# Performance work log

Hardware: AMD Instinct MI355X
Metric: run time of the kernel (lower is better)

## Reference

```python
import jax, jax.numpy as jnp
import numpy as np

SEQ, BATCH, IN = 512, 256, 15
H1, H2, FC_HID, NUM_CLASSES = 512, 512, 64, 1


def setup_inputs() -> dict:
    key = jax.random.key(0)
    ks = jax.random.split(key, 14)
    def u(k, shape, fan_in):
        b = 1.0 / np.sqrt(fan_in)
        return jax.random.uniform(k, shape, jnp.float32, -b, b)
    return {
        "x": jax.random.normal(ks[0], (SEQ, BATCH, IN), jnp.float32),
        # PyTorch LSTM params, gate order i,f,g,o stacked along dim 0
        "W_ih1": u(ks[1], (4 * H1, IN), H1),
        "W_hh1": u(ks[2], (4 * H1, H1), H1),
        "b_ih1": u(ks[3], (4 * H1,), H1),
        "b_hh1": u(ks[4], (4 * H1,), H1),
        "W_ih2": u(ks[5], (4 * H2, H1), H2),
        "W_hh2": u(ks[6], (4 * H2, H2), H2),
        "b_ih2": u(ks[7], (4 * H2,), H2),
        "b_hh2": u(ks[8], (4 * H2,), H2),
        "fc1_w": u(ks[9], (FC_HID, H2), H2),
        "fc1_b": u(ks[10], (FC_HID,), H2),
        "fc_w": u(ks[11], (NUM_CLASSES, FC_HID), FC_HID),
        "fc_b": u(ks[12], (NUM_CLASSES,), FC_HID),
    }


def _lstm_cell(x_t, h, c, W_ih, W_hh, b_ih, b_hh):
    # gates: [B, 4H], PyTorch gate order i, f, g, o
    g = x_t @ W_ih.T + b_ih + h @ W_hh.T + b_hh
    i, f, gg, o = jnp.split(g, 4, axis=-1)
    c_new = jax.nn.sigmoid(f) * c + jax.nn.sigmoid(i) * jnp.tanh(gg)
    h_new = jax.nn.sigmoid(o) * jnp.tanh(c_new)
    return h_new, c_new


def reference(x, W_ih1, W_hh1, b_ih1, b_hh1, W_ih2, W_hh2, b_ih2, b_hh2,
              fc1_w, fc1_b, fc_w, fc_b):
    S, B, _ = x.shape
    init = (jnp.zeros((B, H1), x.dtype), jnp.zeros((B, H1), x.dtype),
            jnp.zeros((B, H2), x.dtype), jnp.zeros((B, H2), x.dtype))

    def step(carry, x_t):
        h1, c1, h2, c2 = carry
        h1, c1 = _lstm_cell(x_t, h1, c1, W_ih1, W_hh1, b_ih1, b_hh1)
        h2, c2 = _lstm_cell(h1, h2, c2, W_ih2, W_hh2, b_ih2, b_hh2)
        return (h1, c1, h2, c2), None

    (h1, c1, h2, c2), _ = jax.lax.scan(step, init, x)
    # MLP head on final-timestep top-layer hidden state; `out += out` doubles it
    hn = jax.nn.relu(h2)
    out = jax.nn.relu(hn @ fc1_w.T + fc1_b)
    out = out @ fc_w.T + fc_b
    return out + out
```

## Files before the change

kernel.cpp:

```cpp
#include <hip/hip_runtime.h>
#include <cstdint>
#include <cstddef>

typedef __attribute__((ext_vector_type(8))) short short8;
typedef __attribute__((ext_vector_type(4))) float floatx4;

constexpr int kSeq = 512;
constexpr int kBatch = 256;
constexpr int kIn = 15;
constexpr int kH = 512;
constexpr int kG = 4 * kH;
constexpr size_t kHSlot = (size_t)kBatch * kH;
constexpr size_t kShmemBytes = 131072 + 4096;

__device__ __forceinline__ unsigned short f2bf(float f) {
    union { float f; unsigned u; } v; v.f = f;
    unsigned u = v.u;
    return (unsigned short)((u + 0x7fffu + ((u >> 16) & 1u)) >> 16);
}

__device__ __forceinline__ float sigm(float x) { return 1.0f / (1.0f + __expf(-x)); }
__device__ __forceinline__ float tanh_(float x) { return 1.0f - 2.0f / (1.0f + __expf(2.0f * x)); }

#define LLC_LOAD16(A, P)                                                      \
    asm volatile(                                                             \
        "global_load_dwordx4 %0, %16, off sc0 sc1\n\t"                        \
        "global_load_dwordx4 %1, %16, off offset:64 sc0 sc1\n\t"              \
        "global_load_dwordx4 %2, %16, off offset:128 sc0 sc1\n\t"             \
        "global_load_dwordx4 %3, %16, off offset:192 sc0 sc1\n\t"             \
        "global_load_dwordx4 %4, %16, off offset:256 sc0 sc1\n\t"             \
        "global_load_dwordx4 %5, %16, off offset:320 sc0 sc1\n\t"             \
        "global_load_dwordx4 %6, %16, off offset:384 sc0 sc1\n\t"             \
        "global_load_dwordx4 %7, %16, off offset:448 sc0 sc1\n\t"             \
        "global_load_dwordx4 %8, %16, off offset:512 sc0 sc1\n\t"             \
        "global_load_dwordx4 %9, %16, off offset:576 sc0 sc1\n\t"             \
        "global_load_dwordx4 %10, %16, off offset:640 sc0 sc1\n\t"            \
        "global_load_dwordx4 %11, %16, off offset:704 sc0 sc1\n\t"            \
        "global_load_dwordx4 %12, %16, off offset:768 sc0 sc1\n\t"            \
        "global_load_dwordx4 %13, %16, off offset:832 sc0 sc1\n\t"            \
        "global_load_dwordx4 %14, %16, off offset:896 sc0 sc1\n\t"            \
        "global_load_dwordx4 %15, %16, off offset:960 sc0 sc1\n\t"            \
        "s_waitcnt vmcnt(0)"                                                  \
        : "=&v"((A)[0]), "=&v"((A)[1]), "=&v"((A)[2]), "=&v"((A)[3]),         \
          "=&v"((A)[4]), "=&v"((A)[5]), "=&v"((A)[6]), "=&v"((A)[7]),         \
          "=&v"((A)[8]), "=&v"((A)[9]), "=&v"((A)[10]), "=&v"((A)[11]),       \
          "=&v"((A)[12]), "=&v"((A)[13]), "=&v"((A)[14]), "=&v"((A)[15])      \
        : "v"(P) : "memory")

#define LLC_STORE16(P, V)                                                     \
    asm volatile("global_store_dwordx4 %0, %1, off sc0 sc1"                   \
                 :: "v"(P), "v"(V) : "memory")

__device__ __forceinline__ void waitf(const int* flags, int tgt, int lane, int& fc) {
    if (tgt <= 0) return;
    bool watch = (lane < 32);
    if (__all(!watch || fc >= tgt)) return;
    for (;;) {
        if (watch && fc < tgt)
            fc = __hip_atomic_load(flags + lane * 16,
                                   __ATOMIC_RELAXED, __HIP_MEMORY_SCOPE_AGENT);
        if (__all(!watch || fc >= tgt)) return;
        __builtin_amdgcn_s_sleep(1);
    }
}

__global__ void k_conv(const float* __restrict__ src, unsigned short* __restrict__ dst, int n) {
    int i = blockIdx.x * blockDim.x + threadIdx.x;
    if (i < n) dst[i] = f2bf(src[i]);
}

__global__ void k_conv_pad(const float* __restrict__ src, unsigned short* __restrict__ dst, int rows) {
    int i = blockIdx.x * blockDim.x + threadIdx.x;
    if (i >= rows * 32) return;
    int r = i >> 5, k = i & 31;
    dst[i] = (k < kIn) ? f2bf(src[r * kIn + k]) : (unsigned short)0;
}

__global__ __launch_bounds__(256) void k_persist(
    const unsigned short* __restrict__ whh1b,
    const unsigned short* __restrict__ wih1b,
    const unsigned short* __restrict__ wih2b,
    const unsigned short* __restrict__ whh2b,
    const unsigned short* __restrict__ xb,
    const float* __restrict__ bih1, const float* __restrict__ bhh1,
    const float* __restrict__ bih2, const float* __restrict__ bhh2,
    unsigned short* __restrict__ h1r,
    unsigned short* __restrict__ h2r,
    float* __restrict__ h2f,
    int* __restrict__ flags)
{
    extern __shared__ unsigned short lw[];
    const int bid = blockIdx.x;
    const int g = bid & 3;
    const int role = bid >> 2;
    const bool is2 = role >= 32;
    const int rid = role & 31;
    const int j0 = rid << 4;
    const int tid = (int)threadIdx.x;
    const int wave = tid >> 6;
    const int lane = tid & 63;
    const int lcol = lane & 15;
    const int quad = lane >> 4;
    const int m0 = (g << 6) + wave * 16;
    const int arow = m0 + lcol;
    const int koff = quad * 8;

    int* f1 = flags + g * 1024;
    int* f2 = f1 + 512;
    int* myflag = (is2 ? f2 : f1) + rid * 16;
    unsigned short* scr = lw + 65536 + wave * 384;

    if (!is2) {
        for (int i = tid; i < 4096; i += 256) {
            int ln = i >> 6, gg = ln >> 4, u = ln & 15;
            int c = i & 63, kk = c >> 2, qd = c & 3;
            *(short8*)&lw[((gg * 16 + kk) << 9) + ((qd * 16 + u) << 3)] =
                *(const short8*)&whh1b[(size_t)((gg << 9) + j0 + u) * kH + c * 8];
        }
        for (int i = tid; i < 256; i += 256) {
            int ln = i >> 2, gg = ln >> 4, u = ln & 15;
            int qd = i & 3;
            *(short8*)&lw[((64 + gg) << 9) + ((qd * 16 + u) << 3)] =
                *(const short8*)&wih1b[((gg << 9) + j0 + u) * 32 + qd * 8];
        }
    } else {
        for (int i = tid; i < 4096; i += 256) {
            int ln = i >> 6, gg = ln >> 4, u = ln & 15;
            int c = i & 63, kk = c >> 2, qd = c & 3;
            int dst = ((gg * 16 + kk) << 9) + ((qd * 16 + u) << 3);
            size_t src = (size_t)((gg << 9) + j0 + u) * kH + c * 8;
            *(short8*)&lw[dst] = *(const short8*)&wih2b[src];
            *(short8*)&lw[dst + (64 << 9)] = *(const short8*)&whh2b[src];
        }
    }
    float bsum[4];
#pragma unroll
    for (int gg = 0; gg < 4; ++gg) {
        int n = (gg << 9) + j0 + lcol;
        bsum[gg] = is2 ? (bih2[n] + bhh2[n]) : (bih1[n] + bhh1[n]);
    }
    __syncthreads();

    float creg[4] = {0.f, 0.f, 0.f, 0.f};
    int fc1 = 0, fc2 = 0;

    if (!is2) {
        for (int s = 0; s < kSeq; ++s) {
            floatx4 acc[4];
#pragma unroll
            for (int gg = 0; gg < 4; ++gg)
                acc[gg] = (floatx4){bsum[gg], bsum[gg], bsum[gg], bsum[gg]};

            short8 ax = *(const short8*)(xb + ((size_t)s * kBatch + arow) * 32 + koff);

            if (wave == 0) waitf(f1, s, lane, fc1);
            __syncthreads();

            const unsigned short* hp = h1r + ((size_t)((s + 3) & 3)) * kHSlot
                                       + (size_t)arow * kH + koff;
            short8 a[16];
            LLC_LOAD16(a, hp);
#pragma unroll
            for (int kk = 0; kk < 16; ++kk) {
#pragma unroll
                for (int gg = 0; gg < 4; ++gg) {
                    short8 b = *(const short8*)&lw[((gg * 16 + kk) << 9) + (lane << 3)];
                    acc[gg] = __builtin_amdgcn_mfma_f32_16x16x32_bf16(a[kk], b, acc[gg], 0, 0, 0);
                }
            }
#pragma unroll
            for (int gg = 0; gg < 4; ++gg) {
                short8 b = *(const short8*)&lw[((64 + gg) << 9) + (lane << 3)];
                acc[gg] = __builtin_amdgcn_mfma_f32_16x16x32_bf16(ax, b, acc[gg], 0, 0, 0);
            }

            if (wave == 0) waitf(f2, s - 2, lane, fc2);
            __syncthreads();

            unsigned short* hw = h1r + ((size_t)(s & 3)) * kHSlot;
#pragma unroll
            for (int r = 0; r < 4; ++r) {
                int row = quad * 4 + r;
                float gi = acc[0][r], gf = acc[1][r], ggv = acc[2][r], go = acc[3][r];
                float cn = sigm(gf) * creg[r] + sigm(gi) * tanh_(ggv);
                float hn = sigm(go) * tanh_(cn);
                creg[r] = cn;
                scr[row * 24 + lcol] = f2bf(hn);
            }
            __syncthreads();
            if (lane < 32) {
                int row = lane >> 1, seg = lane & 1;
                short8 v = *(short8*)&scr[row * 24 + seg * 8];
                unsigned short* gp = hw + (size_t)(m0 + row) * kH + j0 + seg * 8;
                LLC_STORE16(gp, v);
            }
            __builtin_amdgcn_s_waitcnt(0);
            __syncthreads();
            if (tid == 0)
                __hip_atomic_store(myflag, s + 1,
                                   __ATOMIC_RELAXED, __HIP_MEMORY_SCOPE_AGENT);
        }
    } else {
        for (int u = 0; u < kSeq; ++u) {
            floatx4 acc[4];
#pragma unroll
            for (int gg = 0; gg < 4; ++gg)
                acc[gg] = (floatx4){bsum[gg], bsum[gg], bsum[gg], bsum[gg]};

            if (wave == 0) waitf(f2, u, lane, fc2);
            __syncthreads();

            const unsigned short* hp2 = h2r + ((size_t)((u + 1) & 1)) * kHSlot
                                        + (size_t)arow * kH + koff;
            short8 a[16];
            LLC_LOAD16(a, hp2);
#pragma unroll
            for (int kk = 0; kk < 16; ++kk) {
#pragma unroll
                for (int gg = 0; gg < 4; ++gg) {
                    short8 b = *(const short8*)&lw[((64 + gg * 16 + kk) << 9) + (lane << 3)];
                    acc[gg] = __builtin_amdgcn_mfma_f32_16x16x32_bf16(a[kk], b, acc[gg], 0, 0, 0);
                }
            }

            if (wave == 0) waitf(f1, u + 1, lane, fc1);
            __syncthreads();

            const unsigned short* hp1 = h1r + ((size_t)(u & 3)) * kHSlot
                                        + (size_t)arow * kH + koff;
            LLC_LOAD16(a, hp1);
#pragma unroll
            for (int kk = 0; kk < 16; ++kk) {
#pragma unroll
                for (int gg = 0; gg < 4; ++gg) {
                    short8 b = *(const short8*)&lw[((gg * 16 + kk) << 9) + (lane << 3)];
                    acc[gg] = __builtin_amdgcn_mfma_f32_16x16x32_bf16(a[kk], b, acc[gg], 0, 0, 0);
                }
            }

            unsigned short* hw = h2r + ((size_t)(u & 1)) * kHSlot;
            const int j = j0 + lcol;
#pragma unroll
            for (int r = 0; r < 4; ++r) {
                int row = quad * 4 + r;
                float gi = acc[0][r], gf = acc[1][r], ggv = acc[2][r], go = acc[3][r];
                float cn = sigm(gf) * creg[r] + sigm(gi) * tanh_(ggv);
                float hn = sigm(go) * tanh_(cn);
                creg[r] = cn;
                scr[row * 24 + lcol] = f2bf(hn);
                if (u == kSeq - 1) h2f[(size_t)(m0 + row) * kH + j] = hn;
            }
            __syncthreads();
            if (lane < 32) {
                int row = lane >> 1, seg = lane & 1;
                short8 v = *(short8*)&scr[row * 24 + seg * 8];
                unsigned short* gp = hw + (size_t)(m0 + row) * kH + j0 + seg * 8;
                LLC_STORE16(gp, v);
            }
            __builtin_amdgcn_s_waitcnt(0);
            __syncthreads();
            if (tid == 0)
                __hip_atomic_store(myflag, u + 1,
                                   __ATOMIC_RELAXED, __HIP_MEMORY_SCOPE_AGENT);
        }
    }
}

__global__ __launch_bounds__(64) void k_head(
    const float* __restrict__ h2f, const float* __restrict__ fc1w,
    const float* __restrict__ fc1b, const float* __restrict__ fcw,
    const float* __restrict__ fcb, float* __restrict__ out)
{
    int m = blockIdx.x;
    int j = threadIdx.x;
    const float* hr = h2f + (size_t)m * kH;
    const float* wr = fc1w + (size_t)j * kH;
    float sacc = 0.f;
    for (int k = 0; k < kH; ++k) sacc += fmaxf(hr[k], 0.f) * wr[k];
    float rv = fmaxf(sacc + fc1b[j], 0.f) * fcw[j];
#pragma unroll
    for (int off = 32; off >= 1; off >>= 1) rv += __shfl_down(rv, off);
    if (j == 0) out[m] = 2.0f * (rv + fcb[0]);
}

extern "C" void kernel_launch(void* const* d_in, const int* in_sizes, int n_in,
                              void* d_out, int out_size, void* d_ws, size_t ws_size,
                              hipStream_t stream) {
    const float* x    = (const float*)d_in[0];
    const float* Wih1 = (const float*)d_in[1];
    const float* Whh1 = (const float*)d_in[2];
    const float* bih1 = (const float*)d_in[3];
    const float* bhh1 = (const float*)d_in[4];
    const float* Wih2 = (const float*)d_in[5];
    const float* Whh2 = (const float*)d_in[6];
    const float* bih2 = (const float*)d_in[7];
    const float* bhh2 = (const float*)d_in[8];
    const float* fc1w = (const float*)d_in[9];
    const float* fc1b = (const float*)d_in[10];
    const float* fcw  = (const float*)d_in[11];
    const float* fcb  = (const float*)d_in[12];
    float* out = (float*)d_out;

    char* p = (char*)d_ws;
    auto take = [&](size_t bytes) -> char* {
        char* r = p;
        p += (bytes + 255) & ~(size_t)255;
        return r;
    };
    unsigned short* whh1b = (unsigned short*)take((size_t)kG * kH * 2);
    unsigned short* wih2b = (unsigned short*)take((size_t)kG * kH * 2);
    unsigned short* whh2b = (unsigned short*)take((size_t)kG * kH * 2);
    unsigned short* wih1b = (unsigned short*)take((size_t)kG * 32 * 2);
    unsigned short* xb    = (unsigned short*)take((size_t)kSeq * kBatch * 32 * 2);
    char* state = p;
    unsigned short* h1r = (unsigned short*)take(4 * kHSlot * 2);
    unsigned short* h2r = (unsigned short*)take(2 * kHSlot * 2);
    int* flags = (int*)take(16384);
    size_t state_bytes = (size_t)((char*)flags + 16384 - state);
    float* h2f = (float*)take((size_t)kBatch * kH * 4);

    hipMemsetAsync(state, 0, state_bytes, stream);

    int n = kG * kH;
    k_conv<<<(n + 255) / 256, 256, 0, stream>>>(Whh1, whh1b, n);
    k_conv<<<(n + 255) / 256, 256, 0, stream>>>(Wih2, wih2b, n);
    k_conv<<<(n + 255) / 256, 256, 0, stream>>>(Whh2, whh2b, n);
    k_conv_pad<<<(kG * 32 + 255) / 256, 256, 0, stream>>>(Wih1, wih1b, kG);
    k_conv_pad<<<(kSeq * kBatch * 32 + 255) / 256, 256, 0, stream>>>(x, xb, kSeq * kBatch);

    hipFuncSetAttribute((const void*)k_persist,
                        hipFuncAttributeMaxDynamicSharedMemorySize, (int)kShmemBytes);
    void* args[] = {&whh1b, &wih1b, &wih2b, &whh2b, &xb,
                    (void*)&bih1, (void*)&bhh1, (void*)&bih2, (void*)&bhh2,
                    &h1r, &h2r, &h2f, &flags};
    hipError_t e = hipLaunchCooperativeKernel((const void*)k_persist, dim3(256), dim3(256),
                                              args, (unsigned)kShmemBytes, stream);
    if (e != hipSuccess) {
        k_persist<<<256, 256, kShmemBytes, stream>>>(
            whh1b, wih1b, wih2b, whh2b, xb, bih1, bhh1, bih2, bhh2,
            h1r, h2r, h2f, flags);
    }

    k_head<<<kBatch, 64, 0, stream>>>(h2f, fc1w, fc1b, fcw, fcb, out);
}
```

Before: 4.258 ms.

## Use 17-slot hidden-state rings and periodic barriers to loosen layer coupling

Both hidden-state buffers become 17-slot rings instead of 4-slot and 2-slot buffers. This lets layer 1 run up to 16 steps ahead of layer 2, and a joint wait on both layers' flags every 16 steps replaces the per-step back-pressure wait. The inline-asm cache-bypassing loads (sc0 sc1) become plain loads, with an agent-scope acquire fence added only at the periodic barrier. That fence pattern may leave stale cached h values between barriers, a correctness risk. The modulo-17 indexing adds a little integer work and the rings use more workspace.

```diff
diff --git a/kernel.cpp b/kernel.cpp
--- a/kernel.cpp
+++ b/kernel.cpp
@@ -10,6 +10,7 @@
 constexpr int kIn = 15;
 constexpr int kH = 512;
 constexpr int kG = 4 * kH;
+constexpr int kRing = 17;
 constexpr size_t kHSlot = (size_t)kBatch * kH;
 constexpr size_t kShmemBytes = 131072 + 4096;
 
@@ -21,31 +22,6 @@
 
 __device__ __forceinline__ float sigm(float x) { return 1.0f / (1.0f + __expf(-x)); }
 __device__ __forceinline__ float tanh_(float x) { return 1.0f - 2.0f / (1.0f + __expf(2.0f * x)); }
-
-#define LLC_LOAD16(A, P)                                                      \
-    asm volatile(                                                             \
-        "global_load_dwordx4 %0, %16, off sc0 sc1\n\t"                        \
-        "global_load_dwordx4 %1, %16, off offset:64 sc0 sc1\n\t"              \
-        "global_load_dwordx4 %2, %16, off offset:128 sc0 sc1\n\t"             \
-        "global_load_dwordx4 %3, %16, off offset:192 sc0 sc1\n\t"             \
-        "global_load_dwordx4 %4, %16, off offset:256 sc0 sc1\n\t"             \
-        "global_load_dwordx4 %5, %16, off offset:320 sc0 sc1\n\t"             \
-        "global_load_dwordx4 %6, %16, off offset:384 sc0 sc1\n\t"             \
-        "global_load_dwordx4 %7, %16, off offset:448 sc0 sc1\n\t"             \
-        "global_load_dwordx4 %8, %16, off offset:512 sc0 sc1\n\t"             \
-        "global_load_dwordx4 %9, %16, off offset:576 sc0 sc1\n\t"             \
-        "global_load_dwordx4 %10, %16, off offset:640 sc0 sc1\n\t"            \
-        "global_load_dwordx4 %11, %16, off offset:704 sc0 sc1\n\t"            \
-        "global_load_dwordx4 %12, %16, off offset:768 sc0 sc1\n\t"            \
-        "global_load_dwordx4 %13, %16, off offset:832 sc0 sc1\n\t"            \
-        "global_load_dwordx4 %14, %16, off offset:896 sc0 sc1\n\t"            \
-        "global_load_dwordx4 %15, %16, off offset:960 sc0 sc1\n\t"            \
-        "s_waitcnt vmcnt(0)"                                                  \
-        : "=&v"((A)[0]), "=&v"((A)[1]), "=&v"((A)[2]), "=&v"((A)[3]),         \
-          "=&v"((A)[4]), "=&v"((A)[5]), "=&v"((A)[6]), "=&v"((A)[7]),         \
-          "=&v"((A)[8]), "=&v"((A)[9]), "=&v"((A)[10]), "=&v"((A)[11]),       \
-          "=&v"((A)[12]), "=&v"((A)[13]), "=&v"((A)[14]), "=&v"((A)[15])      \
-        : "v"(P) : "memory")
 
 #define LLC_STORE16(P, V)                                                     \
     asm volatile("global_store_dwordx4 %0, %1, off sc0 sc1"                   \
@@ -146,6 +122,11 @@
 
     if (!is2) {
         for (int s = 0; s < kSeq; ++s) {
+            if ((s & 15) == 0) {
+                if (wave == 0) { waitf(f1, s, lane, fc1); waitf(f2, s, lane, fc2); }
+                __syncthreads();
+                __builtin_amdgcn_fence(__ATOMIC_ACQUIRE, "agent");
+            }
             floatx4 acc[4];
 #pragma unroll
             for (int gg = 0; gg < 4; ++gg)
@@ -156,10 +137,11 @@
             if (wave == 0) waitf(f1, s, lane, fc1);
             __syncthreads();
 
-            const unsigned short* hp = h1r + ((size_t)((s + 3) & 3)) * kHSlot
+            const unsigned short* hp = h1r + (size_t)((s + 16) % kRing) * kHSlot
                                        + (size_t)arow * kH + koff;
             short8 a[16];
-            LLC_LOAD16(a, hp);
+#pragma unroll
+            for (int kk = 0; kk < 16; ++kk) a[kk] = *(const short8*)(hp + kk * 32);
 #pragma unroll
             for (int kk = 0; kk < 16; ++kk) {
 #pragma unroll
@@ -174,10 +156,7 @@
                 acc[gg] = __builtin_amdgcn_mfma_f32_16x16x32_bf16(ax, b, acc[gg], 0, 0, 0);
             }
 
-            if (wave == 0) waitf(f2, s - 2, lane, fc2);
-            __syncthreads();
-
-            unsigned short* hw = h1r + ((size_t)(s & 3)) * kHSlot;
+            unsigned short* hw = h1r + (size_t)(s % kRing) * kHSlot;
 #pragma unroll
             for (int r = 0; r < 4; ++r) {
                 int row = quad * 4 + r;
@@ -202,6 +181,11 @@
         }
     } else {
         for (int u = 0; u < kSeq; ++u) {
+            if ((u & 15) == 0) {
+                if (wave == 0) { waitf(f1, u, lane, fc1); waitf(f2, u, lane, fc2); }
+                __syncthreads();
+                __builtin_amdgcn_fence(__ATOMIC_ACQUIRE, "agent");
+            }
             floatx4 acc[4];
 #pragma unroll
             for (int gg = 0; gg < 4; ++gg)
@@ -210,10 +194,11 @@
             if (wave == 0) waitf(f2, u, lane, fc2);
             __syncthreads();
 
-            const unsigned short* hp2 = h2r + ((size_t)((u + 1) & 1)) * kHSlot
+            const unsigned short* hp2 = h2r + (size_t)((u + 16) % kRing) * kHSlot
                                         + (size_t)arow * kH + koff;
             short8 a[16];
-            LLC_LOAD16(a, hp2);
+#pragma unroll
+            for (int kk = 0; kk < 16; ++kk) a[kk] = *(const short8*)(hp2 + kk * 32);
 #pragma unroll
             for (int kk = 0; kk < 16; ++kk) {
 #pragma unroll
@@ -226,9 +211,10 @@
             if (wave == 0) waitf(f1, u + 1, lane, fc1);
             __syncthreads();
 
-            const unsigned short* hp1 = h1r + ((size_t)(u & 3)) * kHSlot
+            const unsigned short* hp1 = h1r + (size_t)(u % kRing) * kHSlot
                                         + (size_t)arow * kH + koff;
-            LLC_LOAD16(a, hp1);
+#pragma unroll
+            for (int kk = 0; kk < 16; ++kk) a[kk] = *(const short8*)(hp1 + kk * 32);
 #pragma unroll
             for (int kk = 0; kk < 16; ++kk) {
 #pragma unroll
@@ -238,7 +224,7 @@
                 }
             }
 
-            unsigned short* hw = h2r + ((size_t)(u & 1)) * kHSlot;
+            unsigned short* hw = h2r + (size_t)(u % kRing) * kHSlot;
             const int j = j0 + lcol;
 #pragma unroll
             for (int r = 0; r < 4; ++r) {
@@ -313,8 +299,8 @@
     unsigned short* wih1b = (unsigned short*)take((size_t)kG * 32 * 2);
     unsigned short* xb    = (unsigned short*)take((size_t)kSeq * kBatch * 32 * 2);
     char* state = p;
-    unsigned short* h1r = (unsigned short*)take(4 * kHSlot * 2);
-    unsigned short* h2r = (unsigned short*)take(2 * kHSlot * 2);
+    unsigned short* h1r = (unsigned short*)take((size_t)kRing * kHSlot * 2);
+    unsigned short* h2r = (unsigned short*)take((size_t)kRing * kHSlot * 2);
     int* flags = (int*)take(16384);
     size_t state_bytes = (size_t)((char*)flags + 16384 - state);
     float* h2f = (float*)take((size_t)kBatch * kH * 4);
```

Result: no change. 4.190 ms (-1.6%).
